# Performance work log

Measured on AMD Instinct MI355X. Metric: run time of the kernel, lower is better.

## Reference

```python
import jax, jax.numpy as jnp
import numpy as np

N = 100000
E = 1250000
F_IN = 64
H = 64


def gcn_conv(x, W, b, src, dst, n):
    """PyG GCNConv: add self loops, symmetric D^-1/2 (A+I) D^-1/2 normalization."""
    h = x @ W  # [N, H]
    # degree after adding self-loops: 1 + in-degree at target nodes
    deg = 1.0 + jax.ops.segment_sum(jnp.ones((src.shape[0],), h.dtype), dst, num_segments=n)
    dinv = jax.lax.rsqrt(deg)  # deg >= 1, safe
    norm = dinv[src] * dinv[dst]  # [E]
    # neighbor aggregation (gather -> scale -> scatter-add) + self-loop term h[i]/deg[i]
    agg = jax.ops.segment_sum(h[src] * norm[:, None], dst, num_segments=n)
    return agg + h * (dinv * dinv)[:, None] + b


def setup_inputs() -> dict:
    key = jax.random.key(0)
    ks = jax.random.split(key, 8)
    x = jax.random.normal(ks[0], (N, F_IN), dtype=jnp.float32)
    edge_index = jax.random.randint(ks[1], (2, E), 0, N, dtype=jnp.int64 if jax.config.jax_enable_x64 else jnp.int32)
    s1 = 1.0 / np.sqrt(F_IN)
    s2 = 1.0 / np.sqrt(H)
    W1 = jax.random.uniform(ks[2], (F_IN, H), jnp.float32, -s1, s1)
    b1 = jnp.zeros((H,), jnp.float32)
    W2 = jax.random.uniform(ks[3], (H, H), jnp.float32, -s2, s2)
    b2 = jnp.zeros((H,), jnp.float32)
    Wo = jax.random.uniform(ks[4], (H, 1), jnp.float32, -s2, s2)
    bo = jax.random.uniform(ks[5], (1,), jnp.float32, -s2, s2)
    return {"x": x, "edge_index": edge_index, "W1": W1, "b1": b1, "W2": W2, "b2": b2, "Wo": Wo, "bo": bo}


def reference(x, edge_index, W1, b1, W2, b2, Wo, bo):
    src, dst = edge_index[0], edge_index[1]
    h = jax.nn.relu(gcn_conv(x, W1, b1, src, dst, N))
    h = jax.nn.relu(gcn_conv(h, W2, b2, src, dst, N))
    return h @ Wo + bo  # [N, 1]
```

## Files before the change

kernel.cpp:

```cpp
#include <hip/hip_runtime.h>


typedef float v2f __attribute__((ext_vector_type(2)));

constexpr int NB_SHIFT = 8;
constexpr int BUCK_NODES = 1 << NB_SHIFT;
constexpr int CAP = 5120;
constexpr int CHUNK = 4096;
constexpr int STPB = 512;

__global__ __launch_bounds__(512) void k_init(int* __restrict__ gcur, int nbuck,
                                              unsigned short* __restrict__ dummyRow) {
    int t = threadIdx.x;
    if (t < nbuck) gcur[t] = 0;
    if (t < 64) dummyRow[t] = 0;
}

__global__ __launch_bounds__(STPB) void k_bsort(const int* __restrict__ src,
                                                const int* __restrict__ dst, int E, int nbuck,
                                                int* __restrict__ gcur,
                                                unsigned* __restrict__ packed) {
    __shared__ int shStart[512];
    __shared__ int shCur[512];
    __shared__ int shOff[512];
    __shared__ unsigned stage[CHUNK];
    __shared__ unsigned short sbkt[CHUNK];
    const int tid = threadIdx.x;
    const int base = blockIdx.x * CHUNK;
    const int end = min(base + CHUNK, E);
    shCur[tid] = 0;
    __syncthreads();
    for (int e = base + tid; e < end; e += STPB)
        atomicAdd(&shCur[dst[e] >> NB_SHIFT], 1);
    __syncthreads();
    int v = shCur[tid];
    shStart[tid] = v;
    __syncthreads();
    for (int s = 1; s < 512; s <<= 1) {
        int a = (tid >= s) ? shStart[tid - s] : 0;
        __syncthreads();
        shStart[tid] += a;
        __syncthreads();
    }
    int exc = shStart[tid] - v;
    shStart[tid] = exc;
    shCur[tid] = exc;
    if (tid < nbuck) shOff[tid] = tid * CAP + ((v > 0) ? atomicAdd(&gcur[tid], v) : 0);
    __syncthreads();
    for (int e = base + tid; e < end; e += STPB) {
        int s = src[e];
        int d = dst[e];
        int b = d >> NB_SHIFT;
        int slot = atomicAdd(&shCur[b], 1);
        stage[slot] = ((unsigned)(d & (BUCK_NODES - 1)) << 17) | (unsigned)s;
        sbkt[slot] = (unsigned short)b;
    }
    __syncthreads();
    int cnt = end - base;
    for (int i = tid; i < cnt; i += STPB) {
        int b = sbkt[i];
        packed[shOff[b] + (i - shStart[b])] = stage[i];
    }
}

__global__ __launch_bounds__(512) void k_csr(const unsigned* __restrict__ packed,
                                             const int* __restrict__ gcur, int n,
                                             int* __restrict__ csr, int2* __restrict__ rowinfo,
                                             float* __restrict__ dinv) {
    __shared__ int cnt[BUCK_NODES];
    __shared__ int scn[BUCK_NODES];
    __shared__ int cur[BUCK_NODES];
    const int tid = threadIdx.x;
    const int e0 = blockIdx.x * CAP;
    const int e1 = e0 + gcur[blockIdx.x];
    if (tid < BUCK_NODES) cnt[tid] = 0;
    __syncthreads();
    for (int e = e0 + tid; e < e1; e += 512)
        atomicAdd(&cnt[packed[e] >> 17], 1);
    __syncthreads();
    int v = (tid < BUCK_NODES) ? cnt[tid] : 0;
    int pad = (v + 2) & ~1;
    if (tid < BUCK_NODES) scn[tid] = pad;
    __syncthreads();
    for (int s = 1; s < BUCK_NODES; s <<= 1) {
        int add = (tid >= s && tid < BUCK_NODES) ? scn[tid - s] : 0;
        __syncthreads();
        if (tid < BUCK_NODES) scn[tid] += add;
        __syncthreads();
    }
    int start = 0;
    if (tid < BUCK_NODES) {
        start = e0 + scn[tid] - pad;
        cur[tid] = start;
        int node = blockIdx.x * BUCK_NODES + tid;
        if (node < n) {
            rowinfo[node] = make_int2(start, pad);
            dinv[node] = rsqrtf(1.0f + (float)v);
        }
    }
    __syncthreads();
    for (int e = e0 + tid; e < e1; e += 512) {
        unsigned p = packed[e];
        int pos = atomicAdd(&cur[p >> 17], 1);
        csr[pos] = (int)(p & 0x1FFFFu);
    }
    __syncthreads();
    if (tid < BUCK_NODES) {
        int node = blockIdx.x * BUCK_NODES + tid;
        csr[start + v] = (node < n) ? node : n;
        for (int p = v + 1; p < pad; ++p) csr[start + p] = n;
    }
}

__global__ __launch_bounds__(256) void k_gemm64bf(const float* __restrict__ A,
                                                  const float* __restrict__ W,
                                                  const float* __restrict__ dinv,
                                                  unsigned short* __restrict__ out,
                                                  int n) {
    const int lane = threadIdx.x & 63;
    const int wave = threadIdx.x >> 6;
    float wcol[64];
#pragma unroll
    for (int k = 0; k < 64; ++k) wcol[k] = W[k * 64 + lane];
    int base = blockIdx.x * 64;
    for (int r = wave; r < 64; r += 4) {
        int row = base + r;
        if (row >= n) break;
        int urow = __builtin_amdgcn_readfirstlane(row);
        const float* Ar = A + (size_t)urow * 64;
        float acc = 0.0f;
#pragma unroll
        for (int k = 0; k < 64; ++k) acc = fmaf(Ar[k], wcol[k], acc);
        float val = acc * dinv[urow];
        unsigned u = __float_as_uint(val);
        u = (u + 0x7FFFu + ((u >> 16) & 1u)) >> 16;
        out[(size_t)urow * 64 + lane] = (unsigned short)u;
    }
}

__device__ __forceinline__ v2f bf2(unsigned u) {
    v2f r;
    r.x = __uint_as_float(u << 16);
    r.y = __uint_as_float(u & 0xFFFF0000u);
    return r;
}

template <bool LAST>
__global__ __launch_bounds__(256) void k_aggregate(
    const uint4* __restrict__ g4,
    const int2* __restrict__ rowinfo, const int* __restrict__ csr,
    const float* __restrict__ dinv, const float* __restrict__ bias,
    const float* __restrict__ Wo, const float* __restrict__ bo,
    float* __restrict__ outRow, float* __restrict__ outHead, int n) {
    int w = (blockIdx.x * blockDim.x + threadIdx.x) >> 6;
    int lane = threadIdx.x & 63;
    const int s = lane >> 4;
    const int grp = (lane >> 3) & 1;
    const int q = lane & 7;
    int node = 4 * w + s;
    const bool valid = node < n;
    int2 ri = valid ? rowinfo[node] : make_int2(0, 0);
    const int e = ri.x;
    const int rnds = ri.y >> 1;
    int rm = rnds;
    rm = max(rm, __shfl_xor(rm, 16, 64));
    rm = max(rm, __shfl_xor(rm, 32, 64));
    v2f a0v = {0.f, 0.f}, a1v = {0.f, 0.f}, a2v = {0.f, 0.f}, a3v = {0.f, 0.f};
    int r = 0;
    for (; r + 4 <= rm; r += 4) {
        int c0 = csr[e + 2 * r + grp];
        int c1 = csr[e + 2 * r + 2 + grp];
        int c2 = csr[e + 2 * r + 4 + grp];
        int c3 = csr[e + 2 * r + 6 + grp];
        int i0 = (r < rnds) ? c0 : n;
        int i1 = (r + 1 < rnds) ? c1 : n;
        int i2 = (r + 2 < rnds) ? c2 : n;
        int i3 = (r + 3 < rnds) ? c3 : n;
        uint4 x0 = g4[(size_t)i0 * 8 + q];
        uint4 x1 = g4[(size_t)i1 * 8 + q];
        uint4 x2 = g4[(size_t)i2 * 8 + q];
        uint4 x3 = g4[(size_t)i3 * 8 + q];
        a0v += bf2(x0.x); a1v += bf2(x0.y); a2v += bf2(x0.z); a3v += bf2(x0.w);
        a0v += bf2(x1.x); a1v += bf2(x1.y); a2v += bf2(x1.z); a3v += bf2(x1.w);
        a0v += bf2(x2.x); a1v += bf2(x2.y); a2v += bf2(x2.z); a3v += bf2(x2.w);
        a0v += bf2(x3.x); a1v += bf2(x3.y); a2v += bf2(x3.z); a3v += bf2(x3.w);
    }
    for (; r < rm; ++r) {
        int c0 = csr[e + 2 * r + grp];
        int i0 = (r < rnds) ? c0 : n;
        uint4 x0 = g4[(size_t)i0 * 8 + q];
        a0v += bf2(x0.x); a1v += bf2(x0.y); a2v += bf2(x0.z); a3v += bf2(x0.w);
    }
    v2f keep0 = grp ? a2v : a0v;
    v2f keep1 = grp ? a3v : a1v;
    v2f send0 = grp ? a0v : a2v;
    v2f send1 = grp ? a1v : a3v;
    keep0.x += __shfl_xor(send0.x, 8, 64);
    keep0.y += __shfl_xor(send0.y, 8, 64);
    keep1.x += __shfl_xor(send1.x, 8, 64);
    keep1.y += __shfl_xor(send1.y, 8, 64);
    const int base = 8 * q + 4 * grp;
    float dv = valid ? dinv[node] : 0.f;
    float4 bb = *(const float4*)&bias[base];
    float4 vv;
    vv.x = fmaxf(fmaf(dv, keep0.x, bb.x), 0.f);
    vv.y = fmaxf(fmaf(dv, keep0.y, bb.y), 0.f);
    vv.z = fmaxf(fmaf(dv, keep1.x, bb.z), 0.f);
    vv.w = fmaxf(fmaf(dv, keep1.y, bb.w), 0.f);
    if constexpr (LAST) {
        float4 ww = *(const float4*)&Wo[base];
        float p = vv.x * ww.x + vv.y * ww.y + vv.z * ww.z + vv.w * ww.w;
#pragma unroll
        for (int m = 1; m <= 8; m <<= 1) p += __shfl_xor(p, m, 64);
        if ((lane & 15) == 0 && valid) outHead[node] = p + bo[0];
    } else {
        if (valid) *(float4*)&outRow[(size_t)node * 64 + base] = vv;
    }
}

extern "C" void kernel_launch(void* const* d_in, const int* in_sizes, int n_in,
                              void* d_out, int out_size, void* d_ws, size_t ws_size,
                              hipStream_t stream) {
    const float* x  = (const float*)d_in[0];
    const int*   ei = (const int*)d_in[1];
    const float* W1 = (const float*)d_in[2];
    const float* b1 = (const float*)d_in[3];
    const float* W2 = (const float*)d_in[4];
    const float* b2 = (const float*)d_in[5];
    const float* Wo = (const float*)d_in[6];
    const float* bo = (const float*)d_in[7];
    float* out = (float*)d_out;

    const int n = in_sizes[0] / 64;
    const int E = in_sizes[1] / 2;
    const int* src = ei;
    const int* dst = ei + E;

    const int nbuck = (n + BUCK_NODES - 1) >> NB_SHIFT;
    const int nchunks = (E + CHUNK - 1) / CHUNK;

    char* ws = (char*)d_ws;
    size_t off = 0;
    auto alloc = [&](size_t bytes) -> void* {
        void* p = ws + off;
        off += (bytes + 255) & ~(size_t)255;
        return p;
    };
    const size_t slabBytes = (size_t)nbuck * CAP * 4 + 4096;
    const size_t hBytes    = (size_t)n * 64 * 4;
    const size_t gBytes    = (size_t)(n + 1) * 64 * 2;
    float*          dinv    = (float*)alloc((size_t)n * 4);
    int*            gcur    = (int*)alloc((size_t)nbuck * 4);
    int2*           rowinfo = (int2*)alloc((size_t)n * 8);
    int*            csr     = (int*)alloc(slabBytes);
    char*           regionA = (char*)alloc(hBytes > slabBytes ? hBytes : slabBytes);
    unsigned short* gBf     = (unsigned short*)alloc(gBytes);
    unsigned* packed = (unsigned*)regionA;
    float*    bufH   = (float*)regionA;

    k_init<<<1, 512, 0, stream>>>(gcur, nbuck, gBf + (size_t)n * 64);

    k_bsort<<<nchunks, STPB, 0, stream>>>(src, dst, E, nbuck, gcur, packed);
    k_csr<<<nbuck, 512, 0, stream>>>(packed, gcur, n, csr, rowinfo, dinv);

    const int gemmGrid = (n + 63) / 64;
    const int nodeGrid = (n + 15) / 16;

    k_gemm64bf<<<gemmGrid, 256, 0, stream>>>(x, W1, dinv, gBf, n);
    k_aggregate<false><<<nodeGrid, 256, 0, stream>>>((const uint4*)gBf, rowinfo, csr,
                                                     dinv, b1, nullptr, nullptr,
                                                     bufH, nullptr, n);
    k_gemm64bf<<<gemmGrid, 256, 0, stream>>>(bufH, W2, dinv, gBf, n);
    k_aggregate<true><<<nodeGrid, 256, 0, stream>>>((const uint4*)gBf, rowinfo, csr,
                                                    dinv, b2, Wo, bo,
                                                    nullptr, out, n);
}
```

Before: 136.2 us.

## Split each node's CSR neighbor list into two source-index halves for gather locality

The CSR build now keys edges by destination node and by whether the source lies in the lower or upper half of the node range. Each node gets two padded segments, with the self-loop placed in the half that owns it, and rowinfo grows to int4 to hold both ranges. The aggregation kernel walks the lower-half segment first and then the upper-half segment, so concurrently running waves tend to gather from a smaller slice of the bf16 feature table and get better L2 reuse. In exchange it adds more padding slots per node, a larger rowinfo array, a 512-entry scan instead of 256 in the CSR kernel, and a second loop with extra shuffles per node.

```diff
diff --git a/kernel.cpp b/kernel.cpp
--- a/kernel.cpp
+++ b/kernel.cpp
@@ -65,50 +65,62 @@
 
 __global__ __launch_bounds__(512) void k_csr(const unsigned* __restrict__ packed,
                                              const int* __restrict__ gcur, int n,
-                                             int* __restrict__ csr, int2* __restrict__ rowinfo,
+                                             int* __restrict__ csr, int4* __restrict__ rowinfo,
                                              float* __restrict__ dinv) {
-    __shared__ int cnt[BUCK_NODES];
-    __shared__ int scn[BUCK_NODES];
-    __shared__ int cur[BUCK_NODES];
+    __shared__ int cnt[512];
+    __shared__ int scn[512];
+    __shared__ int cur[512];
+    __shared__ int st [512];
     const int tid = threadIdx.x;
+    const int nHalf = n >> 1;
     const int e0 = blockIdx.x * CAP;
     const int e1 = e0 + gcur[blockIdx.x];
-    if (tid < BUCK_NODES) cnt[tid] = 0;
-    __syncthreads();
-    for (int e = e0 + tid; e < e1; e += 512)
-        atomicAdd(&cnt[packed[e] >> 17], 1);
-    __syncthreads();
-    int v = (tid < BUCK_NODES) ? cnt[tid] : 0;
-    int pad = (v + 2) & ~1;
-    if (tid < BUCK_NODES) scn[tid] = pad;
-    __syncthreads();
-    for (int s = 1; s < BUCK_NODES; s <<= 1) {
-        int add = (tid >= s && tid < BUCK_NODES) ? scn[tid - s] : 0;
-        __syncthreads();
-        if (tid < BUCK_NODES) scn[tid] += add;
-        __syncthreads();
-    }
-    int start = 0;
+    cnt[tid] = 0;
+    __syncthreads();
+    for (int e = e0 + tid; e < e1; e += 512) {
+        unsigned p = packed[e];
+        int key = (int)((p >> 17) << 1) | (((p & 0x1FFFFu) >= (unsigned)nHalf) ? 1 : 0);
+        atomicAdd(&cnt[key], 1);
+    }
+    __syncthreads();
+    int v = cnt[tid];
+    int nodeK = blockIdx.x * BUCK_NODES + (tid >> 1);
+    bool selfHere = (nodeK < n) && (((nodeK >= nHalf) ? 1 : 0) == (tid & 1));
+    int pad = (v + (selfHere ? 1 : 0) + 1) & ~1;
+    scn[tid] = pad;
+    __syncthreads();
+    for (int s = 1; s < 512; s <<= 1) {
+        int add = (tid >= s) ? scn[tid - s] : 0;
+        __syncthreads();
+        scn[tid] += add;
+        __syncthreads();
+    }
+    int start = e0 + scn[tid] - pad;
+    st[tid] = start;
+    cur[tid] = start;
+    __syncthreads();
+    for (int e = e0 + tid; e < e1; e += 512) {
+        unsigned p = packed[e];
+        unsigned s = p & 0x1FFFFu;
+        int key = (int)((p >> 17) << 1) | ((s >= (unsigned)nHalf) ? 1 : 0);
+        int pos = atomicAdd(&cur[key], 1);
+        csr[pos] = (int)s;
+    }
+    __syncthreads();
+    {
+        int endK = (tid < 511) ? st[tid + 1] : (e0 + scn[511]);
+        int p = cur[tid];
+        if (selfHere) csr[p++] = nodeK;
+        for (; p < endK; ++p) csr[p] = n;
+    }
     if (tid < BUCK_NODES) {
-        start = e0 + scn[tid] - pad;
-        cur[tid] = start;
         int node = blockIdx.x * BUCK_NODES + tid;
         if (node < n) {
-            rowinfo[node] = make_int2(start, pad);
-            dinv[node] = rsqrtf(1.0f + (float)v);
+            int sA = st[2 * tid], sB = st[2 * tid + 1];
+            int eB = (2 * tid + 2 < 512) ? st[2 * tid + 2] : (e0 + scn[511]);
+            rowinfo[node] = make_int4(sA, sB - sA, sB, eB - sB);
+            dinv[node] = rsqrtf(1.0f + (float)(cnt[2 * tid] + cnt[2 * tid + 1]));
         }
-    }
-    __syncthreads();
-    for (int e = e0 + tid; e < e1; e += 512) {
-        unsigned p = packed[e];
-        int pos = atomicAdd(&cur[p >> 17], 1);
-        csr[pos] = (int)(p & 0x1FFFFu);
-    }
-    __syncthreads();
-    if (tid < BUCK_NODES) {
-        int node = blockIdx.x * BUCK_NODES + tid;
-        csr[start + v] = (node < n) ? node : n;
-        for (int p = v + 1; p < pad; ++p) csr[start + p] = n;
     }
 }
 
@@ -148,7 +160,7 @@
 template <bool LAST>
 __global__ __launch_bounds__(256) void k_aggregate(
     const uint4* __restrict__ g4,
-    const int2* __restrict__ rowinfo, const int* __restrict__ csr,
+    const int4* __restrict__ rowinfo, const int* __restrict__ csr,
     const float* __restrict__ dinv, const float* __restrict__ bias,
     const float* __restrict__ Wo, const float* __restrict__ bo,
     float* __restrict__ outRow, float* __restrict__ outHead, int n) {
@@ -159,37 +171,40 @@
     const int q = lane & 7;
     int node = 4 * w + s;
     const bool valid = node < n;
-    int2 ri = valid ? rowinfo[node] : make_int2(0, 0);
-    const int e = ri.x;
-    const int rnds = ri.y >> 1;
-    int rm = rnds;
-    rm = max(rm, __shfl_xor(rm, 16, 64));
-    rm = max(rm, __shfl_xor(rm, 32, 64));
+    int4 ri = valid ? rowinfo[node] : make_int4(0, 0, 0, 0);
     v2f a0v = {0.f, 0.f}, a1v = {0.f, 0.f}, a2v = {0.f, 0.f}, a3v = {0.f, 0.f};
-    int r = 0;
-    for (; r + 4 <= rm; r += 4) {
-        int c0 = csr[e + 2 * r + grp];
-        int c1 = csr[e + 2 * r + 2 + grp];
-        int c2 = csr[e + 2 * r + 4 + grp];
-        int c3 = csr[e + 2 * r + 6 + grp];
-        int i0 = (r < rnds) ? c0 : n;
-        int i1 = (r + 1 < rnds) ? c1 : n;
-        int i2 = (r + 2 < rnds) ? c2 : n;
-        int i3 = (r + 3 < rnds) ? c3 : n;
-        uint4 x0 = g4[(size_t)i0 * 8 + q];
-        uint4 x1 = g4[(size_t)i1 * 8 + q];
-        uint4 x2 = g4[(size_t)i2 * 8 + q];
-        uint4 x3 = g4[(size_t)i3 * 8 + q];
-        a0v += bf2(x0.x); a1v += bf2(x0.y); a2v += bf2(x0.z); a3v += bf2(x0.w);
-        a0v += bf2(x1.x); a1v += bf2(x1.y); a2v += bf2(x1.z); a3v += bf2(x1.w);
-        a0v += bf2(x2.x); a1v += bf2(x2.y); a2v += bf2(x2.z); a3v += bf2(x2.w);
-        a0v += bf2(x3.x); a1v += bf2(x3.y); a2v += bf2(x3.z); a3v += bf2(x3.w);
-    }
-    for (; r < rm; ++r) {
-        int c0 = csr[e + 2 * r + grp];
-        int i0 = (r < rnds) ? c0 : n;
-        uint4 x0 = g4[(size_t)i0 * 8 + q];
-        a0v += bf2(x0.x); a1v += bf2(x0.y); a2v += bf2(x0.z); a3v += bf2(x0.w);
+#pragma unroll 2
+    for (int ph = 0; ph < 2; ++ph) {
+        const int e = ph ? ri.z : ri.x;
+        const int rnds = (ph ? ri.w : ri.y) >> 1;
+        int rm = rnds;
+        rm = max(rm, __shfl_xor(rm, 16, 64));
+        rm = max(rm, __shfl_xor(rm, 32, 64));
+        int r = 0;
+        for (; r + 4 <= rm; r += 4) {
+            int c0 = csr[e + 2 * r + grp];
+            int c1 = csr[e + 2 * r + 2 + grp];
+            int c2 = csr[e + 2 * r + 4 + grp];
+            int c3 = csr[e + 2 * r + 6 + grp];
+            int i0 = (r < rnds) ? c0 : n;
+            int i1 = (r + 1 < rnds) ? c1 : n;
+            int i2 = (r + 2 < rnds) ? c2 : n;
+            int i3 = (r + 3 < rnds) ? c3 : n;
+            uint4 x0 = g4[(size_t)i0 * 8 + q];
+            uint4 x1 = g4[(size_t)i1 * 8 + q];
+            uint4 x2 = g4[(size_t)i2 * 8 + q];
+            uint4 x3 = g4[(size_t)i3 * 8 + q];
+            a0v += bf2(x0.x); a1v += bf2(x0.y); a2v += bf2(x0.z); a3v += bf2(x0.w);
+            a0v += bf2(x1.x); a1v += bf2(x1.y); a2v += bf2(x1.z); a3v += bf2(x1.w);
+            a0v += bf2(x2.x); a1v += bf2(x2.y); a2v += bf2(x2.z); a3v += bf2(x2.w);
+            a0v += bf2(x3.x); a1v += bf2(x3.y); a2v += bf2(x3.z); a3v += bf2(x3.w);
+        }
+        for (; r < rm; ++r) {
+            int c0 = csr[e + 2 * r + grp];
+            int i0 = (r < rnds) ? c0 : n;
+            uint4 x0 = g4[(size_t)i0 * 8 + q];
+            a0v += bf2(x0.x); a1v += bf2(x0.y); a2v += bf2(x0.z); a3v += bf2(x0.w);
+        }
     }
     v2f keep0 = grp ? a2v : a0v;
     v2f keep1 = grp ? a3v : a1v;
@@ -251,7 +266,7 @@
     const size_t gBytes    = (size_t)(n + 1) * 64 * 2;
     float*          dinv    = (float*)alloc((size_t)n * 4);
     int*            gcur    = (int*)alloc((size_t)nbuck * 4);
-    int2*           rowinfo = (int2*)alloc((size_t)n * 8);
+    int4*           rowinfo = (int4*)alloc((size_t)n * 16);
     int*            csr     = (int*)alloc(slabBytes);
     char*           regionA = (char*)alloc(hBytes > slabBytes ? hBytes : slabBytes);
     unsigned short* gBf     = (unsigned short*)alloc(gBytes);
```

Result: no change. 138.8 us (+1.9%).
